# Kernel tuning notes

Hardware: AMD Instinct MI355X
Metric: run time of the kernel (lower is better)

Reference implementation:

```python
import jax, jax.numpy as jnp
import numpy as np

PIECES = 64  # self.plane


def _proj(f, w1, b1, w2, b2):
    # Projection: fc2(relu(fc1(f))), final_relu=False
    h = jax.nn.relu(f @ w1 + b1)
    return h @ w2 + b2


def _cf(img, param, pieces):
    # img: [B,3,H,W], param: [B,3,P]
    # total[b,c,h,w] = sum_i clamp(img - i/P, 0, 1/P) * param[b,c,i], then * P / sum_i param
    grid = jnp.arange(pieces, dtype=img.dtype) / pieces            # [P]
    clipped = jnp.clip(img[..., None] - grid, 0.0, 1.0 / pieces)   # [B,3,H,W,P]
    total = jnp.einsum('bchwp,bcp->bchw', clipped, param)
    norm = pieces / (jnp.sum(param, axis=-1) + 1e-30)              # [B,3]
    return total * norm[:, :, None, None]


def setup_inputs() -> dict:
    key = jax.random.key(0)
    ks = jax.random.split(key, 11)
    B, H, W = 8, 256, 256
    s = 0.05
    return {
        'x': jax.random.uniform(ks[0], (B, 3, H, W), jnp.float32),
        'f_feature': jax.random.normal(ks[1], (B, 512), jnp.float32),
        'b_feature': jax.random.normal(ks[2], (B, 512), jnp.float32),
        # stacked weights for [fc_f_1, fc_b_1, fc_f_s, fc_b_s]
        'proj_w1': jax.random.normal(ks[3], (4, 512, 192), jnp.float32) * s,
        'proj_b1': jax.random.normal(ks[4], (4, 192), jnp.float32) * s,
        'proj_w2': jax.random.normal(ks[5], (4, 192, 192), jnp.float32) * s,
        'proj_b2': jax.random.normal(ks[6], (4, 192), jnp.float32) * s,
        'fc_w1': jax.random.normal(ks[7], (576, 192), jnp.float32) * s,
        'fc_b1': jax.random.normal(ks[8], (192,), jnp.float32) * s,
        'fc_w2': jax.random.normal(ks[9], (192, 192), jnp.float32) * s,
        'fc_b2': jax.random.normal(ks[10], (192,), jnp.float32) * s,
    }


def reference(x, f_feature, b_feature, proj_w1, proj_b1, proj_w2, proj_b2,
              fc_w1, fc_b1, fc_w2, fc_b2):
    B = x.shape[0]
    # rgb_to_grayscale with 3 output channels (ITU-R 601 weights)
    gw = jnp.array([0.299, 0.587, 0.114], dtype=x.dtype)
    gray = jnp.broadcast_to(jnp.einsum('bchw,c->bhw', x, gw)[:, None], x.shape)

    # four stacked Projections: inputs [f, b, f, b]
    feats = jnp.stack([f_feature, b_feature, f_feature, b_feature])       # [4,B,512]
    h = jax.nn.relu(jnp.einsum('kbi,kio->kbo', feats, proj_w1) + proj_b1[:, None, :])
    outs = jnp.einsum('kbo,koq->kbq', h, proj_w2) + proj_b2[:, None, :]   # [4,B,192]
    param_f, param_b = outs[0], outs[1]
    param_s = outs[2] + outs[3]

    cat = jnp.concatenate([param_f, param_b, param_s], axis=1)            # [B,576]
    param = _proj(cat, fc_w1, fc_b1, fc_w2, fc_b2)                        # [B,192]

    p_all = param.reshape(B, 3, PIECES)
    p_f = param_f.reshape(B, 3, PIECES)
    p_b = param_b.reshape(B, 3, PIECES)

    return (_cf(x, p_all, PIECES), _cf(gray, p_f, PIECES), _cf(gray, p_b, PIECES))
```

## Files before the change

kernel.cpp:

```cpp
#include <hip/hip_runtime.h>

#define HWSZ 65536
#define PLANE (3 * HWSZ)
#define OUTSTRIDE (8 * PLANE)
#define MAGIC 0x13572468

__global__ __launch_bounds__(384) void k_mlp(
    const float* __restrict__ f, const float* __restrict__ bf,
    const float* __restrict__ pw1, const float* __restrict__ pb1,
    const float* __restrict__ pw2, const float* __restrict__ pb2,
    const float* __restrict__ fw1, const float* __restrict__ fb1,
    const float* __restrict__ fw2, const float* __restrict__ fb2,
    float* __restrict__ ws) {
  __shared__ float smem[2304];
  int t = threadIdx.x, blk = blockIdx.x;

  float* outs  = ws;
  float* hc    = ws + 12288;
  float* param = ws + 13824;
  int* fbase = (int*)(ws + 16384);

  int k = blk >> 3, b = blk & 7;
  {
    int q = t % 48, s = t / 48;
    float* sf  = smem;
    float* red = smem + 512;
    float* sh  = smem + 2048;

    const float* feat = ((k & 1) ? bf : f) + b * 512;
    for (int i = t; i < 512; i += 384) sf[i] = feat[i];
    __syncthreads();

    {
      const float4* w = (const float4*)(pw1 + (size_t)k * (512 * 192));
      float4 acc = {0.f, 0.f, 0.f, 0.f};
      int i0 = s * 64;
      for (int r = 0; r < 4; ++r) {
        float4 wv[16];
#pragma unroll
        for (int j = 0; j < 16; ++j)
          wv[j] = w[(size_t)(i0 + r * 16 + j) * 48 + q];
#pragma unroll
        for (int j = 0; j < 16; ++j) {
          float v = sf[i0 + r * 16 + j];
          acc.x = fmaf(v, wv[j].x, acc.x); acc.y = fmaf(v, wv[j].y, acc.y);
          acc.z = fmaf(v, wv[j].z, acc.z); acc.w = fmaf(v, wv[j].w, acc.w);
        }
      }
      ((float4*)(red + s * 192))[q] = acc;
    }
    __syncthreads();
    if (t < 192) {
      float a = pb1[k * 192 + t];
#pragma unroll
      for (int s2 = 0; s2 < 8; ++s2) a += red[s2 * 192 + t];
      sh[t] = fmaxf(a, 0.f);
    }
    __syncthreads();
    {
      const float4* w = (const float4*)(pw2 + (size_t)k * (192 * 192));
      float4 acc = {0.f, 0.f, 0.f, 0.f};
      int i0 = s * 24;
      for (int r = 0; r < 2; ++r) {
        float4 wv[12];
#pragma unroll
        for (int j = 0; j < 12; ++j)
          wv[j] = w[(size_t)(i0 + r * 12 + j) * 48 + q];
#pragma unroll
        for (int j = 0; j < 12; ++j) {
          float v = sh[i0 + r * 12 + j];
          acc.x = fmaf(v, wv[j].x, acc.x); acc.y = fmaf(v, wv[j].y, acc.y);
          acc.z = fmaf(v, wv[j].z, acc.z); acc.w = fmaf(v, wv[j].w, acc.w);
        }
      }
      ((float4*)(red + s * 192))[q] = acc;
    }
    __syncthreads();
    if (t < 192) {
      float a = pb2[k * 192 + t];
#pragma unroll
      for (int s2 = 0; s2 < 8; ++s2) a += red[s2 * 192 + t];
      outs[(k * 8 + b) * 192 + t] = a;
    }
    __syncthreads();
    if (t == 0) {
      __threadfence();
      atomicExch(&fbase[blk * 16], MAGIC);
    }
  }

  int b2 = blk & 7, c4 = blk >> 3, ob2 = c4 * 48;
  if (t < 4) {
    while (atomicAdd(&fbase[(t * 8 + b2) * 16], 0) != MAGIC)
      __builtin_amdgcn_s_sleep(2);
  }
  __syncthreads();
  if (t == 0) __threadfence();
  __syncthreads();

  {
    int q = t % 12, s = t / 12;
    float* sc  = smem;
    float* red = smem + 576;
    for (int idx = t; idx < 576; idx += 384) {
      float v;
      if (idx < 192)      v = outs[(0 * 8 + b2) * 192 + idx];
      else if (idx < 384) v = outs[(1 * 8 + b2) * 192 + (idx - 192)];
      else                v = outs[(2 * 8 + b2) * 192 + (idx - 384)] +
                              outs[(3 * 8 + b2) * 192 + (idx - 384)];
      sc[idx] = v;
    }
    const float4* w = (const float4*)fw1;
    float4 acc = {0.f, 0.f, 0.f, 0.f};
    int i0 = s * 18;
    {
      float4 wv[18];
#pragma unroll
      for (int j = 0; j < 18; ++j)
        wv[j] = w[(size_t)(i0 + j) * 48 + (ob2 >> 2) + q];
      __syncthreads();
#pragma unroll
      for (int j = 0; j < 18; ++j) {
        float v = sc[i0 + j];
        acc.x = fmaf(v, wv[j].x, acc.x); acc.y = fmaf(v, wv[j].y, acc.y);
        acc.z = fmaf(v, wv[j].z, acc.z); acc.w = fmaf(v, wv[j].w, acc.w);
      }
    }
    ((float4*)(red + s * 48))[q] = acc;
    __syncthreads();
    if (t < 48) {
      float a = fb1[ob2 + t];
#pragma unroll
      for (int s2 = 0; s2 < 32; ++s2) a += red[s2 * 48 + t];
      hc[b2 * 192 + ob2 + t] = fmaxf(a, 0.f);
    }
    __syncthreads();
    if (t == 0) {
      __threadfence();
      atomicExch(&fbase[(64 + blk) * 16], MAGIC);
    }
  }

  if (t < 4) {
    while (atomicAdd(&fbase[(64 + t * 8 + b2) * 16], 0) != MAGIC)
      __builtin_amdgcn_s_sleep(2);
  }
  __syncthreads();
  if (t == 0) __threadfence();
  __syncthreads();

  {
    int q = t % 12, s = t / 12;
    float* sh  = smem;
    float* red = smem + 576;
    if (t < 192) sh[t] = hc[b2 * 192 + t];
    const float4* w = (const float4*)fw2;
    float4 acc = {0.f, 0.f, 0.f, 0.f};
    int i0 = s * 6;
    {
      float4 wv[6];
#pragma unroll
      for (int j = 0; j < 6; ++j)
        wv[j] = w[(size_t)(i0 + j) * 48 + (ob2 >> 2) + q];
      __syncthreads();
#pragma unroll
      for (int j = 0; j < 6; ++j) {
        float v = sh[i0 + j];
        acc.x = fmaf(v, wv[j].x, acc.x); acc.y = fmaf(v, wv[j].y, acc.y);
        acc.z = fmaf(v, wv[j].z, acc.z); acc.w = fmaf(v, wv[j].w, acc.w);
      }
    }
    ((float4*)(red + s * 48))[q] = acc;
    __syncthreads();
    if (t < 48) {
      float a = fb2[ob2 + t];
#pragma unroll
      for (int s2 = 0; s2 < 32; ++s2) a += red[s2 * 48 + t];
      param[b2 * 192 + ob2 + t] = a;
    }
  }
}

__global__ __launch_bounds__(256) void k_render(
    const float* __restrict__ x, const float* __restrict__ ws,
    float* __restrict__ out) {
  int b = blockIdx.y, t = threadIdx.x;
  int wave = t >> 6, lane = t & 63;
  const float* outs  = ws;
  const float* param = ws + 13824;
  __shared__ float2 tab[576];

  int s4 = blockIdx.x * 256 + t;
  const float* xb = x + (size_t)b * PLANE;
  float4 vr = ((const float4*)(xb))[s4];
  float4 vg = ((const float4*)(xb + HWSZ))[s4];
  float4 vb = ((const float4*)(xb + 2 * HWSZ))[s4];

  for (int cur = wave; cur < 9; cur += 4) {
    int oi = cur / 3, c = cur - oi * 3;
    const float* src = (oi == 0) ? param + b * 192 + c * 64
                                 : outs + ((oi - 1) * 8 + b) * 192 + c * 64;
    float p = src[lane];
    float v = p;
#pragma unroll
    for (int d = 1; d < 64; d <<= 1) {
      float n = __shfl_up(v, d, 64);
      if (lane >= d) v += n;
    }
    float total = __shfl(v, 63, 64);
    float norm = 64.f / (total + 1e-30f);
    tab[cur * 64 + lane] = make_float2((v - p) * 0.015625f * norm, p * norm);
  }
  __syncthreads();

  auto ev = [&](int cur, float v) -> float {
    int k = (int)(v * 64.f);
    k = k < 0 ? 0 : (k > 63 ? 63 : k);
    float2 e = tab[cur * 64 + k];
    float tt = v - (float)k * 0.015625f;
    return fmaf(tt, e.y, e.x);
  };
  auto ev4 = [&](int cur, float4 v) -> float4 {
    float4 r;
    r.x = ev(cur, v.x); r.y = ev(cur, v.y);
    r.z = ev(cur, v.z); r.w = ev(cur, v.w);
    return r;
  };

  float4 gr;
  gr.x = fmaf(0.299f, vr.x, fmaf(0.587f, vg.x, 0.114f * vb.x));
  gr.y = fmaf(0.299f, vr.y, fmaf(0.587f, vg.y, 0.114f * vb.y));
  gr.z = fmaf(0.299f, vr.z, fmaf(0.587f, vg.z, 0.114f * vb.z));
  gr.w = fmaf(0.299f, vr.w, fmaf(0.587f, vg.w, 0.114f * vb.w));

  float* o0 = out + (size_t)b * PLANE;
  float* o1 = out + OUTSTRIDE + (size_t)b * PLANE;
  float* o2 = out + 2 * OUTSTRIDE + (size_t)b * PLANE;

  ((float4*)(o0))[s4]            = ev4(0, vr);
  ((float4*)(o0 + HWSZ))[s4]     = ev4(1, vg);
  ((float4*)(o0 + 2 * HWSZ))[s4] = ev4(2, vb);
  ((float4*)(o1))[s4]            = ev4(3, gr);
  ((float4*)(o1 + HWSZ))[s4]     = ev4(4, gr);
  ((float4*)(o1 + 2 * HWSZ))[s4] = ev4(5, gr);
  ((float4*)(o2))[s4]            = ev4(6, gr);
  ((float4*)(o2 + HWSZ))[s4]     = ev4(7, gr);
  ((float4*)(o2 + 2 * HWSZ))[s4] = ev4(8, gr);
}

extern "C" void kernel_launch(void* const* d_in, const int* in_sizes, int n_in,
                              void* d_out, int out_size, void* d_ws, size_t ws_size,
                              hipStream_t stream) {
  const float* x   = (const float*)d_in[0];
  const float* f   = (const float*)d_in[1];
  const float* bf  = (const float*)d_in[2];
  const float* pw1 = (const float*)d_in[3];
  const float* pb1 = (const float*)d_in[4];
  const float* pw2 = (const float*)d_in[5];
  const float* pb2 = (const float*)d_in[6];
  const float* fw1 = (const float*)d_in[7];
  const float* fb1 = (const float*)d_in[8];
  const float* fw2 = (const float*)d_in[9];
  const float* fb2 = (const float*)d_in[10];
  float* out = (float*)d_out;
  float* ws  = (float*)d_ws;

  k_mlp<<<32, 384, 0, stream>>>(f, bf, pw1, pb1, pw2, pb2, fw1, fb1, fw2,
                                fb2, ws);
  dim3 grid(64, 8);
  k_render<<<grid, 256, 0, stream>>>(x, ws, out);
}
```

Measured before the change: 100.1 us.

## Prefetch MLP weights before spin-waits and process two pixel groups per render thread

In the MLP kernel, the fc1 and fc2 weight loads are issued before each inter-block spin-wait, so their global memory latency overlaps the wait instead of following it. The render kernel now handles two float4 pixel groups per thread with half as many blocks. This amortises the per-block table build (prefix scan plus a barrier) over more pixels. The grayscale bin index and fraction are computed once and reused across the six gray channels. The trade-off is higher register pressure from holding the prefetched weights and the doubled input registers, plus fewer render blocks to hide latency.

```diff
diff --git a/kernel.cpp b/kernel.cpp
--- a/kernel.cpp
+++ b/kernel.cpp
@@ -90,6 +90,17 @@
   }
 
   int b2 = blk & 7, c4 = blk >> 3, ob2 = c4 * 48;
+  int q = t % 12, s = t / 12;
+
+  float4 wv1[18];
+  {
+    const float4* w = (const float4*)fw1;
+    int i0 = s * 18;
+#pragma unroll
+    for (int j = 0; j < 18; ++j)
+      wv1[j] = w[(size_t)(i0 + j) * 48 + (ob2 >> 2) + q];
+  }
+
   if (t < 4) {
     while (atomicAdd(&fbase[(t * 8 + b2) * 16], 0) != MAGIC)
       __builtin_amdgcn_s_sleep(2);
@@ -99,7 +110,6 @@
   __syncthreads();
 
   {
-    int q = t % 12, s = t / 12;
     float* sc  = smem;
     float* red = smem + 576;
     for (int idx = t; idx < 576; idx += 384) {
@@ -110,21 +120,14 @@
                               outs[(3 * 8 + b2) * 192 + (idx - 384)];
       sc[idx] = v;
     }
-    const float4* w = (const float4*)fw1;
+    __syncthreads();
     float4 acc = {0.f, 0.f, 0.f, 0.f};
     int i0 = s * 18;
-    {
-      float4 wv[18];
-#pragma unroll
-      for (int j = 0; j < 18; ++j)
-        wv[j] = w[(size_t)(i0 + j) * 48 + (ob2 >> 2) + q];
-      __syncthreads();
-#pragma unroll
-      for (int j = 0; j < 18; ++j) {
-        float v = sc[i0 + j];
-        acc.x = fmaf(v, wv[j].x, acc.x); acc.y = fmaf(v, wv[j].y, acc.y);
-        acc.z = fmaf(v, wv[j].z, acc.z); acc.w = fmaf(v, wv[j].w, acc.w);
-      }
+#pragma unroll
+    for (int j = 0; j < 18; ++j) {
+      float v = sc[i0 + j];
+      acc.x = fmaf(v, wv1[j].x, acc.x); acc.y = fmaf(v, wv1[j].y, acc.y);
+      acc.z = fmaf(v, wv1[j].z, acc.z); acc.w = fmaf(v, wv1[j].w, acc.w);
     }
     ((float4*)(red + s * 48))[q] = acc;
     __syncthreads();
@@ -141,6 +144,15 @@
     }
   }
 
+  float4 wv2[6];
+  {
+    const float4* w = (const float4*)fw2;
+    int i0 = s * 6;
+#pragma unroll
+    for (int j = 0; j < 6; ++j)
+      wv2[j] = w[(size_t)(i0 + j) * 48 + (ob2 >> 2) + q];
+  }
+
   if (t < 4) {
     while (atomicAdd(&fbase[(64 + t * 8 + b2) * 16], 0) != MAGIC)
       __builtin_amdgcn_s_sleep(2);
@@ -150,25 +162,17 @@
   __syncthreads();
 
   {
-    int q = t % 12, s = t / 12;
     float* sh  = smem;
     float* red = smem + 576;
     if (t < 192) sh[t] = hc[b2 * 192 + t];
-    const float4* w = (const float4*)fw2;
+    __syncthreads();
     float4 acc = {0.f, 0.f, 0.f, 0.f};
     int i0 = s * 6;
-    {
-      float4 wv[6];
-#pragma unroll
-      for (int j = 0; j < 6; ++j)
-        wv[j] = w[(size_t)(i0 + j) * 48 + (ob2 >> 2) + q];
-      __syncthreads();
-#pragma unroll
-      for (int j = 0; j < 6; ++j) {
-        float v = sh[i0 + j];
-        acc.x = fmaf(v, wv[j].x, acc.x); acc.y = fmaf(v, wv[j].y, acc.y);
-        acc.z = fmaf(v, wv[j].z, acc.z); acc.w = fmaf(v, wv[j].w, acc.w);
-      }
+#pragma unroll
+    for (int j = 0; j < 6; ++j) {
+      float v = sh[i0 + j];
+      acc.x = fmaf(v, wv2[j].x, acc.x); acc.y = fmaf(v, wv2[j].y, acc.y);
+      acc.z = fmaf(v, wv2[j].z, acc.z); acc.w = fmaf(v, wv2[j].w, acc.w);
     }
     ((float4*)(red + s * 48))[q] = acc;
     __syncthreads();
@@ -190,11 +194,14 @@
   const float* param = ws + 13824;
   __shared__ float2 tab[576];
 
-  int s4 = blockIdx.x * 256 + t;
+  int s4a = blockIdx.x * 512 + t, s4b = s4a + 256;
   const float* xb = x + (size_t)b * PLANE;
-  float4 vr = ((const float4*)(xb))[s4];
-  float4 vg = ((const float4*)(xb + HWSZ))[s4];
-  float4 vb = ((const float4*)(xb + 2 * HWSZ))[s4];
+  float4 vr0 = ((const float4*)(xb))[s4a];
+  float4 vr1 = ((const float4*)(xb))[s4b];
+  float4 vg0 = ((const float4*)(xb + HWSZ))[s4a];
+  float4 vg1 = ((const float4*)(xb + HWSZ))[s4b];
+  float4 vb0 = ((const float4*)(xb + 2 * HWSZ))[s4a];
+  float4 vb1 = ((const float4*)(xb + 2 * HWSZ))[s4b];
 
   for (int cur = wave; cur < 9; cur += 4) {
     int oi = cur / 3, c = cur - oi * 3;
@@ -213,39 +220,61 @@
   }
   __syncthreads();
 
-  auto ev = [&](int cur, float v) -> float {
+  auto idx_of = [&](float v, int& kk, float& tt) {
     int k = (int)(v * 64.f);
     k = k < 0 ? 0 : (k > 63 ? 63 : k);
+    kk = k;
+    tt = v - (float)k * 0.015625f;
+  };
+  auto evk = [&](int cur, int k, float tt) -> float {
     float2 e = tab[cur * 64 + k];
-    float tt = v - (float)k * 0.015625f;
     return fmaf(tt, e.y, e.x);
   };
   auto ev4 = [&](int cur, float4 v) -> float4 {
-    float4 r;
-    r.x = ev(cur, v.x); r.y = ev(cur, v.y);
-    r.z = ev(cur, v.z); r.w = ev(cur, v.w);
+    int k; float tt; float4 r;
+    idx_of(v.x, k, tt); r.x = evk(cur, k, tt);
+    idx_of(v.y, k, tt); r.y = evk(cur, k, tt);
+    idx_of(v.z, k, tt); r.z = evk(cur, k, tt);
+    idx_of(v.w, k, tt); r.w = evk(cur, k, tt);
     return r;
   };
-
-  float4 gr;
-  gr.x = fmaf(0.299f, vr.x, fmaf(0.587f, vg.x, 0.114f * vb.x));
-  gr.y = fmaf(0.299f, vr.y, fmaf(0.587f, vg.y, 0.114f * vb.y));
-  gr.z = fmaf(0.299f, vr.z, fmaf(0.587f, vg.z, 0.114f * vb.z));
-  gr.w = fmaf(0.299f, vr.w, fmaf(0.587f, vg.w, 0.114f * vb.w));
 
   float* o0 = out + (size_t)b * PLANE;
   float* o1 = out + OUTSTRIDE + (size_t)b * PLANE;
   float* o2 = out + 2 * OUTSTRIDE + (size_t)b * PLANE;
 
-  ((float4*)(o0))[s4]            = ev4(0, vr);
-  ((float4*)(o0 + HWSZ))[s4]     = ev4(1, vg);
-  ((float4*)(o0 + 2 * HWSZ))[s4] = ev4(2, vb);
-  ((float4*)(o1))[s4]            = ev4(3, gr);
-  ((float4*)(o1 + HWSZ))[s4]     = ev4(4, gr);
-  ((float4*)(o1 + 2 * HWSZ))[s4] = ev4(5, gr);
-  ((float4*)(o2))[s4]            = ev4(6, gr);
-  ((float4*)(o2 + HWSZ))[s4]     = ev4(7, gr);
-  ((float4*)(o2 + 2 * HWSZ))[s4] = ev4(8, gr);
+  auto process = [&](int s4, float4 vr, float4 vg, float4 vb) {
+    float4 gr;
+    gr.x = fmaf(0.299f, vr.x, fmaf(0.587f, vg.x, 0.114f * vb.x));
+    gr.y = fmaf(0.299f, vr.y, fmaf(0.587f, vg.y, 0.114f * vb.y));
+    gr.z = fmaf(0.299f, vr.z, fmaf(0.587f, vg.z, 0.114f * vb.z));
+    gr.w = fmaf(0.299f, vr.w, fmaf(0.587f, vg.w, 0.114f * vb.w));
+
+    ((float4*)(o0))[s4]            = ev4(0, vr);
+    ((float4*)(o0 + HWSZ))[s4]     = ev4(1, vg);
+    ((float4*)(o0 + 2 * HWSZ))[s4] = ev4(2, vb);
+
+    int kx, ky, kz, kw; float tx, ty, tz, tw;
+    idx_of(gr.x, kx, tx); idx_of(gr.y, ky, ty);
+    idx_of(gr.z, kz, tz); idx_of(gr.w, kw, tw);
+#pragma unroll
+    for (int c = 0; c < 3; ++c) {
+      float4 r;
+      r.x = evk(3 + c, kx, tx); r.y = evk(3 + c, ky, ty);
+      r.z = evk(3 + c, kz, tz); r.w = evk(3 + c, kw, tw);
+      ((float4*)(o1 + c * HWSZ))[s4] = r;
+    }
+#pragma unroll
+    for (int c = 0; c < 3; ++c) {
+      float4 r;
+      r.x = evk(6 + c, kx, tx); r.y = evk(6 + c, ky, ty);
+      r.z = evk(6 + c, kz, tz); r.w = evk(6 + c, kw, tw);
+      ((float4*)(o2 + c * HWSZ))[s4] = r;
+    }
+  };
+
+  process(s4a, vr0, vg0, vb0);
+  process(s4b, vr1, vg1, vb1);
 }
 
 extern "C" void kernel_launch(void* const* d_in, const int* in_sizes, int n_in,
@@ -267,6 +296,6 @@
 
   k_mlp<<<32, 384, 0, stream>>>(f, bf, pw1, pb1, pw2, pb2, fw1, fb1, fw2,
                                 fb2, ws);
-  dim3 grid(64, 8);
+  dim3 grid(32, 8);
   k_render<<<grid, 256, 0, stream>>>(x, ws, out);
 }
```

Result: no change. 98.87 us (-1.2%).
